# Optimization experiments

Hardware: AMD Instinct MI355X
Metric: run time of the kernel (lower is better)

## Reference

```python
import jax, jax.numpy as jnp
import numpy as np
from jax import lax

V, E, H, K = 50257, 256, 256, 3
T, B, S = 1024, 32, 1024


def setup_inputs() -> dict:
    key = jax.random.key(0)
    ks = jax.random.split(key, 10)
    inp = {
        "source": jax.random.randint(ks[0], (T, B), 0, V),
        "target": jax.random.randint(ks[1], (T, B), 0, V),
        "enc_attn": jax.random.normal(ks[2], (B, S, H), jnp.float32),
        "source_seq_out": jax.random.normal(ks[3], (B, S, 2 * H), jnp.float32),
        "emb": jax.random.normal(ks[4], (V, E), jnp.float32) * 0.02,
        "affine_w": jax.random.normal(ks[5], (2 * H, E), jnp.float32) * 0.02,
        "affine_b": jnp.zeros((2 * H,), jnp.float32),
        "conv_w": jax.random.normal(ks[6], (2 * H, 1, K, 2 * H), jnp.float32) * 0.02,
        "conv_b": jnp.zeros((2 * H,), jnp.float32),
        "map_w": jax.random.normal(ks[7], (2 * H, H), jnp.float32) * 0.02,
        "map_b": jnp.zeros((2 * H,), jnp.float32),
    }
    return inp


def reference(source, target, enc_attn, source_seq_out, emb, affine_w, affine_b,
              conv_w, conv_b, map_w, map_b):
    # source is unused by the original forward (kept for signature fidelity)
    x = emb[target]                                   # [T, B, E]
    x = x @ affine_w.T + affine_b                     # [T, B, 2H]
    x = jnp.transpose(x, (1, 0, 2))                   # [B, T, 2H]  (.t() swaps dims 0,1)
    x = x[:, None, :, :]                              # [B, 1, T, 2H]
    # conv2d: out_ch=2H, kernel=(K, 2H), padding=(K-1, 0) -> [B, 2H, T+K-1, 1]
    y = lax.conv_general_dilated(
        x, conv_w, window_strides=(1, 1),
        padding=((K - 1, K - 1), (0, 0)),
        dimension_numbers=("NCHW", "OIHW", "NCHW"))
    y = y + conv_b[None, :, None, None]
    y = y[:, :, : y.shape[2] - K, :]                  # narrow -> length L = T - 1 (faithful)
    y = jax.nn.relu(y)
    y = jnp.transpose(y[..., 0], (0, 2, 1))           # [B, L, 2H]
    A, Bg = y[..., :H], y[..., H:]                    # GLU split
    dec_attn = A * jax.nn.softmax(Bg, axis=-1)        # [B, L, H]
    dec_attn2 = dec_attn @ map_w.T + map_b            # [B, L, 2H]
    scores = jnp.einsum("blh,bsh->bls", dec_attn, enc_attn)   # [B, L, S]
    attn = jax.nn.softmax(scores, axis=-1)
    attns = jnp.einsum("bls,bsd->bld", attn, source_seq_out)  # [B, L, 2H]
    return dec_attn2 + attns
```

## Files before the change

kernel.cpp:

```cpp
#include <hip/hip_runtime.h>
#include <stdint.h>


typedef __bf16 bf16x8_t __attribute__((ext_vector_type(8)));
typedef float  f32x4_t  __attribute__((ext_vector_type(4)));
typedef unsigned short u16x8 __attribute__((ext_vector_type(8)));

#define DEV __device__ __forceinline__

DEV unsigned short f2bf(float f) {
  union { float f; unsigned u; } v; v.f = f;
  unsigned r = v.u + 0x7fffu + ((v.u >> 16) & 1u);
  return (unsigned short)(r >> 16);
}
DEV float bf2f(unsigned short u) {
  union { unsigned u; float f; } v; v.u = ((unsigned)u) << 16;
  return v.f;
}

DEV void gload_lds16(const void* g, void* l) {
  __builtin_amdgcn_global_load_lds((const __attribute__((address_space(1))) void*)g,
                                   (__attribute__((address_space(3))) void*)l, 16, 0, 0);
}

DEV void vm_bar8() { asm volatile("s_waitcnt vmcnt(8)" ::: "memory"); __builtin_amdgcn_s_barrier(); }
DEV void vm_bar4() { asm volatile("s_waitcnt vmcnt(4)" ::: "memory"); __builtin_amdgcn_s_barrier(); }
DEV void vm_bar0() { asm volatile("s_waitcnt vmcnt(0)" ::: "memory"); __builtin_amdgcn_s_barrier(); }
DEV void lgkm_bar() { asm volatile("s_waitcnt lgkmcnt(0)" ::: "memory"); __builtin_amdgcn_s_barrier(); }

DEV void stage32(unsigned short* Ld, int tid,
                 const unsigned short* a0, const unsigned short* a1,
                 const unsigned short* b0, const unsigned short* b1, int tt) {
  const int o = tt * 32;
  gload_lds16(a0 + o, Ld + tid * 8);
  gload_lds16(a1 + o, Ld + (tid + 256) * 8);
  gload_lds16(b0 + o, Ld + 4096 + tid * 8);
  gload_lds16(b1 + o, Ld + 4096 + (tid + 256) * 8);
}

DEV void gemm_step32(const unsigned short* Ld, int wr, int wc, int ln, int qsw,
                     f32x4_t (&acc)[4][4]) {
  bf16x8_t af[4], bff[4];
#pragma unroll
  for (int x = 0; x < 4; ++x) {
    af[x]  = *(const bf16x8_t*)(Ld + (wr * 64 + x * 16 + ln) * 32 + qsw);
    bff[x] = *(const bf16x8_t*)(Ld + 4096 + (wc * 64 + x * 16 + ln) * 32 + qsw);
  }
  __builtin_amdgcn_s_setprio(1);
#pragma unroll
  for (int mt = 0; mt < 4; ++mt)
#pragma unroll
    for (int nt = 0; nt < 4; ++nt)
      acc[mt][nt] = __builtin_amdgcn_mfma_f32_16x16x32_bf16(af[mt], bff[nt], acc[mt][nt], 0, 0, 0);
  __builtin_amdgcn_s_setprio(0);
}

__global__ void zero_k(unsigned short* p) { p[threadIdx.x] = 0; }

__global__ __launch_bounds__(256) void zero_rows_k(float* p) {
  int i = (blockIdx.x * 256 + threadIdx.x) * 4;
  *(float4*)(p + i) = make_float4(0.f, 0.f, 0.f, 0.f);
}

__global__ __launch_bounds__(256) void cvt_bf16_k(const float* __restrict__ src,
                                                  unsigned short* __restrict__ dst,
                                                  int n) {
  int i = (blockIdx.x * 256 + threadIdx.x) * 4;
  if (i >= n) return;
  float4 v = *(const float4*)(src + i);
  ushort4 o;
  o.x = f2bf(v.x); o.y = f2bf(v.y); o.z = f2bf(v.z); o.w = f2bf(v.w);
  *(ushort4*)(dst + i) = o;
}

__global__ __launch_bounds__(256) void cvt_transpose_v_k(const float* __restrict__ src,
                                                         unsigned short* __restrict__ dst) {
  __shared__ float tile[64][65];
  const int b = blockIdx.z, s0 = blockIdx.x * 64, d0 = blockIdx.y * 64;
  const int tid = threadIdx.x;
  const int cs = (tid & 15) * 4;
  const int rs = tid >> 4;
  const float* p = src + ((size_t)b * 1024 + s0) * 512 + d0;
#pragma unroll
  for (int rr = 0; rr < 4; ++rr) {
    const int s = rs + rr * 16;
    float4 v = *(const float4*)(p + (size_t)s * 512 + cs);
    tile[s][cs] = v.x; tile[s][cs + 1] = v.y;
    tile[s][cs + 2] = v.z; tile[s][cs + 3] = v.w;
  }
  __syncthreads();
  const int ch = tid & 7;
  const int dd0 = tid >> 3;
#pragma unroll
  for (int it = 0; it < 2; ++it) {
    const int dd = dd0 + it * 32;
    u16x8 o;
#pragma unroll
    for (int j = 0; j < 8; ++j) o[j] = f2bf(tile[ch * 8 + j][dd]);
    *(u16x8*)(dst + ((size_t)b * 512 + d0 + dd) * 1024 + s0 + ch * 8) = o;
  }
}

__global__ __launch_bounds__(256) void embed_affine_k(const int* __restrict__ tgt,
                                                      const float* __restrict__ emb,
                                                      const unsigned short* __restrict__ awb,
                                                      const float* __restrict__ ab,
                                                      unsigned short* __restrict__ X) {
  constexpr int AP = 264;
  __shared__ unsigned short xs[32 * AP];
  const int r0 = blockIdx.x * 32;
  const int tid = threadIdx.x;
  for (int idx = tid; idx < 32 * 64; idx += 256) {
    int r = idx >> 6, c4 = (idx & 63) * 4;
    int row = tgt[r0 + r];
    float4 v = *(const float4*)&emb[(size_t)row * 256 + c4];
    ushort4 o;
    o.x = f2bf(v.x); o.y = f2bf(v.y); o.z = f2bf(v.z); o.w = f2bf(v.w);
    *(ushort4*)&xs[r * AP + c4] = o;
  }
  __syncthreads();
  const int lane = tid & 63, w = tid >> 6, q = lane >> 4, ln = lane & 15;
  f32x4_t acc[2][8];
#pragma unroll
  for (int mt = 0; mt < 2; ++mt)
#pragma unroll
    for (int nt = 0; nt < 8; ++nt) acc[mt][nt] = (f32x4_t){0.f, 0.f, 0.f, 0.f};
  for (int kk = 0; kk < 256; kk += 32) {
    bf16x8_t a[2], bb[8];
#pragma unroll
    for (int mt = 0; mt < 2; ++mt)
      a[mt] = *(const bf16x8_t*)(xs + (mt * 16 + ln) * AP + kk + q * 8);
#pragma unroll
    for (int nt = 0; nt < 8; ++nt) {
      int n = ((w * 8 + nt) << 4) + ln;
      bb[nt] = *(const bf16x8_t*)(awb + ((size_t)n << 8) + kk + q * 8);
    }
#pragma unroll
    for (int mt = 0; mt < 2; ++mt)
#pragma unroll
      for (int nt = 0; nt < 8; ++nt)
        acc[mt][nt] = __builtin_amdgcn_mfma_f32_16x16x32_bf16(a[mt], bb[nt], acc[mt][nt], 0, 0, 0);
  }
#pragma unroll
  for (int nt = 0; nt < 8; ++nt) {
    const int o = ((w * 8 + nt) << 4) + ln;
    const float bias = ab[o];
#pragma unroll
    for (int mt = 0; mt < 2; ++mt)
#pragma unroll
      for (int r = 0; r < 4; ++r) {
        int rid = r0 + mt * 16 + q * 4 + r;
        int t = rid >> 5, b = rid & 31;
        X[(((size_t)(b * 1024 + t)) << 9) + o] = f2bf(acc[mt][nt][r] + bias);
      }
  }
}

__global__ __launch_bounds__(256, 3) void conv_gemm_k(const unsigned short* __restrict__ X,
                                                      const unsigned short* __restrict__ Wc,
                                                      const float* __restrict__ cb,
                                                      const unsigned short* __restrict__ zbuf,
                                                      unsigned short* __restrict__ Y) {
  __shared__ unsigned short tb[3][8192];
  const int bid = blockIdx.x;
  const int mtile = ((bid >> 5) << 3) | (bid & 7);
  const int ntile = (bid >> 3) & 3;
  const int b  = mtile >> 3;
  const int l0 = (mtile & 7) << 7;
  const int n0 = ntile << 7;
  const int tid = threadIdx.x;
  const int w = tid >> 6, lane = tid & 63, q = lane >> 4, ln = lane & 15;
  const int wr = w >> 1, wc = w & 1;
  const int qsw = (q ^ (ln & 3)) << 3;

  const int r0g = tid >> 2, r1g = (tid + 256) >> 2;
  const int cg = tid & 3;
  const int c0g = ((cg ^ (r0g & 3)) << 3);
  const int c1g = ((cg ^ (r1g & 3)) << 3);

  const unsigned short* Xb = X + ((size_t)b << 19);
  const int lr0 = l0 + r0g - 2;
  const int lr1 = l0 + r1g - 2;
  const int tmin0 = (lr0 >= 0) ? 0 : (lr0 == -1 ? 16 : 32);
  const unsigned short* a0 = Xb + ((long)lr0 * 512 + c0g);
  const unsigned short* a1 = Xb + ((long)lr1 * 512 + c1g);
  const unsigned short* b0 = Wc + (size_t)(n0 + r0g) * 1536 + c0g;
  const unsigned short* b1 = Wc + (size_t)(n0 + r1g) * 1536 + c1g;

  auto STG = [&](unsigned short* Ld, int tt) {
    const int o = tt * 32;
    const unsigned short* sA0 = (tt >= tmin0) ? (a0 + o) : (zbuf + c0g);
    gload_lds16(sA0, Ld + tid * 8);
    gload_lds16(a1 + o, Ld + (tid + 256) * 8);
    gload_lds16(b0 + o, Ld + 4096 + tid * 8);
    gload_lds16(b1 + o, Ld + 4096 + (tid + 256) * 8);
  };

  f32x4_t acc[4][4];
#pragma unroll
  for (int mt = 0; mt < 4; ++mt)
#pragma unroll
    for (int nt = 0; nt < 4; ++nt) acc[mt][nt] = (f32x4_t){0.f, 0.f, 0.f, 0.f};

  unsigned short *p0 = tb[0], *p1 = tb[1], *p2 = tb[2];
  STG(p0, 0);
  STG(p1, 1);

  for (int t = 0; t < 48; ++t) {
    if (t + 2 < 48) { STG(p2, t + 2); vm_bar8(); }
    else if (t + 1 < 48) vm_bar4();
    else vm_bar0();
    gemm_step32(p0, wr, wc, ln, qsw, acc);
    lgkm_bar();
    unsigned short* tmp = p0; p0 = p1; p1 = p2; p2 = tmp;
  }

#pragma unroll
  for (int nt = 0; nt < 4; ++nt) {
    const int o = n0 + wc * 64 + nt * 16 + ln;
    const float bias = cb[o];
#pragma unroll
    for (int mt = 0; mt < 4; ++mt)
#pragma unroll
      for (int r = 0; r < 4; ++r) {
        const int l = l0 + wr * 64 + mt * 16 + q * 4 + r;
        float v = acc[mt][nt][r] + bias;
        Y[(((size_t)b * 1024 + l) << 9) + o] = f2bf(v > 0.f ? v : 0.f);
      }
  }
}

__global__ __launch_bounds__(256) void glu_k(const unsigned short* __restrict__ Y,
                                             unsigned short* __restrict__ dec) {
  const int row = blockIdx.x * 4 + (threadIdx.x >> 6);
  const int lane = threadIdx.x & 63;
  const unsigned short* p = Y + ((size_t)row << 9);
  ushort4 av = *(const ushort4*)(p + lane * 4);
  ushort4 gv = *(const ushort4*)(p + 256 + lane * 4);
  float e0 = __expf(bf2f(gv.x)), e1 = __expf(bf2f(gv.y));
  float e2 = __expf(bf2f(gv.z)), e3 = __expf(bf2f(gv.w));
  float s = e0 + e1 + e2 + e3;
#pragma unroll
  for (int off = 32; off > 0; off >>= 1) s += __shfl_xor(s, off);
  float inv = 1.f / s;
  ushort4 o;
  o.x = f2bf(bf2f(av.x) * e0 * inv);
  o.y = f2bf(bf2f(av.y) * e1 * inv);
  o.z = f2bf(bf2f(av.z) * e2 * inv);
  o.w = f2bf(bf2f(av.w) * e3 * inv);
  *(ushort4*)(dec + ((size_t)row << 8) + lane * 4) = o;
}

__global__ __launch_bounds__(256, 3) void attn_s_k(const unsigned short* __restrict__ dec,
                                                   const unsigned short* __restrict__ enc,
                                                   unsigned short* __restrict__ P,
                                                   float* __restrict__ rows) {
  __shared__ unsigned short tb[3][8192];
  const int bid = blockIdx.x;
  const int wg = ((bid & 7) << 8) + (bid >> 3);
  const int ntile = wg & 7, mtile = wg >> 3;
  const int b = mtile >> 3;
  const int row0 = mtile << 7;
  const int s0 = ntile << 7;
  const int tid = threadIdx.x;
  const int w = tid >> 6, lane = tid & 63, q = lane >> 4, ln = lane & 15;
  const int wr = w >> 1, wc = w & 1;
  const int qsw = (q ^ (ln & 3)) << 3;

  const int r0g = tid >> 2, r1g = (tid + 256) >> 2;
  const int cg = tid & 3;
  const int c0g = ((cg ^ (r0g & 3)) << 3);
  const int c1g = ((cg ^ (r1g & 3)) << 3);

  const unsigned short* Ab = dec + ((size_t)row0 << 8);
  const unsigned short* Bb = enc + ((size_t)b << 18) + ((size_t)s0 << 8);
  const unsigned short* a0 = Ab + (size_t)r0g * 256 + c0g;
  const unsigned short* a1 = Ab + (size_t)r1g * 256 + c1g;
  const unsigned short* b0 = Bb + (size_t)r0g * 256 + c0g;
  const unsigned short* b1 = Bb + (size_t)r1g * 256 + c1g;

  f32x4_t acc[4][4];
#pragma unroll
  for (int mt = 0; mt < 4; ++mt)
#pragma unroll
    for (int nt = 0; nt < 4; ++nt) acc[mt][nt] = (f32x4_t){0.f, 0.f, 0.f, 0.f};

  unsigned short *p0 = tb[0], *p1 = tb[1], *p2 = tb[2];
  stage32(p0, tid, a0, a1, b0, b1, 0);
  stage32(p1, tid, a0, a1, b0, b1, 1);

  for (int t = 0; t < 8; ++t) {
    if (t + 2 < 8) { stage32(p2, tid, a0, a1, b0, b1, t + 2); vm_bar8(); }
    else if (t + 1 < 8) vm_bar4();
    else vm_bar0();
    gemm_step32(p0, wr, wc, ln, qsw, acc);
    lgkm_bar();
    unsigned short* tmp = p0; p0 = p1; p1 = p2; p2 = tmp;
  }

  float rs[4][4];
#pragma unroll
  for (int mt = 0; mt < 4; ++mt)
#pragma unroll
    for (int r = 0; r < 4; ++r) rs[mt][r] = 0.f;
#pragma unroll
  for (int nt = 0; nt < 4; ++nt) {
    const int col = s0 + wc * 64 + nt * 16 + ln;
#pragma unroll
    for (int mt = 0; mt < 4; ++mt)
#pragma unroll
      for (int r = 0; r < 4; ++r) {
        const int row = row0 + wr * 64 + mt * 16 + q * 4 + r;
        float e = __expf(acc[mt][nt][r]);
        rs[mt][r] += e;
        P[((size_t)row << 10) + col] = f2bf(e);
      }
  }
#pragma unroll
  for (int mt = 0; mt < 4; ++mt)
#pragma unroll
    for (int r = 0; r < 4; ++r) {
      float v = rs[mt][r];
      v += __shfl_xor(v, 1); v += __shfl_xor(v, 2);
      v += __shfl_xor(v, 4); v += __shfl_xor(v, 8);
      if (ln == 0)
        atomicAdd(&rows[row0 + wr * 64 + mt * 16 + q * 4 + r], v);
    }
}

__global__ __launch_bounds__(256, 3) void attn_pv_k(const unsigned short* __restrict__ P,
                                                    const unsigned short* __restrict__ vt,
                                                    const unsigned short* __restrict__ dec,
                                                    const unsigned short* __restrict__ mw,
                                                    const float* __restrict__ rows,
                                                    const float* __restrict__ mb,
                                                    float* __restrict__ out) {
  __shared__ unsigned short tb[3][8192];
  const int bid = blockIdx.x;
  const int wg = ((bid & 7) << 7) + (bid >> 3);
  const int ntile = wg & 3, mtile = wg >> 2;
  const int b = mtile >> 3;
  const int row0 = mtile << 7;
  const int d0 = ntile << 7;
  const int tid = threadIdx.x;
  const int w = tid >> 6, lane = tid & 63, q = lane >> 4, ln = lane & 15;
  const int wr = w >> 1, wc = w & 1;
  const int qsw = (q ^ (ln & 3)) << 3;

  const int r0g = tid >> 2, r1g = (tid + 256) >> 2;
  const int cg = tid & 3;
  const int c0g = ((cg ^ (r0g & 3)) << 3);
  const int c1g = ((cg ^ (r1g & 3)) << 3);

  const unsigned short* A1 = P + ((size_t)row0 << 10);
  const unsigned short* B1 = vt + ((size_t)b << 19) + ((size_t)d0 << 10);
  const unsigned short* A2 = dec + ((size_t)row0 << 8);
  const unsigned short* B2 = mw + ((size_t)d0 << 8);
  const unsigned short* a10 = A1 + (size_t)r0g * 1024 + c0g;
  const unsigned short* a11 = A1 + (size_t)r1g * 1024 + c1g;
  const unsigned short* b10 = B1 + (size_t)r0g * 1024 + c0g;
  const unsigned short* b11 = B1 + (size_t)r1g * 1024 + c1g;
  const unsigned short* a20 = A2 + (size_t)r0g * 256 + c0g;
  const unsigned short* a21 = A2 + (size_t)r1g * 256 + c1g;
  const unsigned short* b20 = B2 + (size_t)r0g * 256 + c0g;
  const unsigned short* b21 = B2 + (size_t)r1g * 256 + c1g;

  auto STG = [&](unsigned short* Ld, int tt) {
    if (tt < 32) stage32(Ld, tid, a10, a11, b10, b11, tt);
    else         stage32(Ld, tid, a20, a21, b20, b21, tt - 32);
  };

  float rinv[4][4];
#pragma unroll
  for (int mt = 0; mt < 4; ++mt)
#pragma unroll
    for (int r = 0; r < 4; ++r)
      rinv[mt][r] = 1.f / rows[row0 + wr * 64 + mt * 16 + q * 4 + r];

  f32x4_t acc[4][4];
#pragma unroll
  for (int mt = 0; mt < 4; ++mt)
#pragma unroll
    for (int nt = 0; nt < 4; ++nt) acc[mt][nt] = (f32x4_t){0.f, 0.f, 0.f, 0.f};

  unsigned short *p0 = tb[0], *p1 = tb[1], *p2 = tb[2];
  STG(p0, 0);
  STG(p1, 1);

  for (int t = 0; t < 32; ++t) {
    STG(p2, t + 2); vm_bar8();
    gemm_step32(p0, wr, wc, ln, qsw, acc);
    lgkm_bar();
    unsigned short* tmp = p0; p0 = p1; p1 = p2; p2 = tmp;
  }
#pragma unroll
  for (int mt = 0; mt < 4; ++mt)
#pragma unroll
    for (int nt = 0; nt < 4; ++nt)
#pragma unroll
      for (int r = 0; r < 4; ++r) acc[mt][nt][r] *= rinv[mt][r];

  for (int t = 32; t < 40; ++t) {
    if (t + 2 < 40) { STG(p2, t + 2); vm_bar8(); }
    else if (t + 1 < 40) vm_bar4();
    else vm_bar0();
    gemm_step32(p0, wr, wc, ln, qsw, acc);
    lgkm_bar();
    unsigned short* tmp = p0; p0 = p1; p1 = p2; p2 = tmp;
  }

#pragma unroll
  for (int nt = 0; nt < 4; ++nt) {
    const int d = d0 + wc * 64 + nt * 16 + ln;
    const float bias = mb[d];
#pragma unroll
    for (int mt = 0; mt < 4; ++mt)
#pragma unroll
      for (int r = 0; r < 4; ++r) {
        const int row = row0 + wr * 64 + mt * 16 + q * 4 + r;
        const int l = row & 1023;
        if (l < 1023)
          out[((size_t)b * 1023 + l) * 512 + d] = acc[mt][nt][r] + bias;
      }
  }
}

extern "C" void kernel_launch(void* const* d_in, const int* in_sizes, int n_in,
                              void* d_out, int out_size, void* d_ws, size_t ws_size,
                              hipStream_t stream) {
  const int*   target = (const int*)d_in[1];
  const float* enc    = (const float*)d_in[2];
  const float* src    = (const float*)d_in[3];
  const float* emb    = (const float*)d_in[4];
  const float* aw     = (const float*)d_in[5];
  const float* ab     = (const float*)d_in[6];
  const float* cw     = (const float*)d_in[7];
  const float* cb     = (const float*)d_in[8];
  const float* mw     = (const float*)d_in[9];
  const float* mb     = (const float*)d_in[10];
  float* out = (float*)d_out;
  char* ws = (char*)d_ws;

  unsigned short* Xbf  = (unsigned short*)(ws);
  unsigned short* Ybf  = (unsigned short*)(ws + 33554432);
  unsigned short* Pb   = (unsigned short*)(ws);
  unsigned short* dec  = (unsigned short*)(ws + 67108864);
  unsigned short* encb = (unsigned short*)(ws + 83886080);
  unsigned short* vtb  = (unsigned short*)(ws + 100663296);
  unsigned short* wcb  = (unsigned short*)(ws + 134217728);
  float*          rows = (float*)(ws + 134217728);
  unsigned short* mwb  = (unsigned short*)(ws + 135790592);
  unsigned short* awb  = (unsigned short*)(ws + 136052736);

  zero_k<<<1, 512, 0, stream>>>(dec);
  cvt_bf16_k<<<8192, 256, 0, stream>>>(enc, encb, 32 * 1024 * 256);
  cvt_bf16_k<<<768, 256, 0, stream>>>(cw, wcb, 512 * 1536);
  cvt_bf16_k<<<128, 256, 0, stream>>>(mw, mwb, 512 * 256);
  cvt_bf16_k<<<128, 256, 0, stream>>>(aw, awb, 512 * 256);
  cvt_transpose_v_k<<<dim3(16, 8, 32), 256, 0, stream>>>(src, vtb);
  embed_affine_k<<<1024, 256, 0, stream>>>(target, emb, awb, ab, Xbf);
  conv_gemm_k<<<1024, 256, 0, stream>>>(Xbf, wcb, cb, dec, Ybf);
  zero_rows_k<<<32, 256, 0, stream>>>(rows);
  glu_k<<<8192, 256, 0, stream>>>(Ybf, dec);
  attn_s_k<<<2048, 256, 0, stream>>>(dec, encb, Pb, rows);
  attn_pv_k<<<1024, 256, 0, stream>>>(Pb, vtb, dec, mwb, rows, mb, out);
}
```

Baseline: 415.6 us.

## Use 256x256 tiles with 8-wave blocks and 4-stage split A/B pipeline

Both conv_gemm_k and attn_pv_k move from 128x128 tiles with 4 waves to 256x256 tiles with 8 waves per block. LDS staging becomes a 4-buffer ring, with the A and B loads issued separately between two MFMA half-steps, and setprio raised around the MFMA bursts. The goal is more operand reuse per global load and better overlap of loads with matrix math. The costs are larger accumulator register use, 256 blocks instead of 1024 (lower occupancy and tail effects on 256 CUs), and extra barriers per k-step.

```diff
diff --git a/kernel.cpp b/kernel.cpp
--- a/kernel.cpp
+++ b/kernel.cpp
@@ -156,63 +156,84 @@
   }
 }
 
-__global__ __launch_bounds__(256, 3) void conv_gemm_k(const unsigned short* __restrict__ X,
+__global__ __launch_bounds__(512, 2) void conv_gemm_k(const unsigned short* __restrict__ X,
                                                       const unsigned short* __restrict__ Wc,
                                                       const float* __restrict__ cb,
                                                       const unsigned short* __restrict__ zbuf,
                                                       unsigned short* __restrict__ Y) {
-  __shared__ unsigned short tb[3][8192];
+  __shared__ unsigned short lds[4][16384];
+  const int tid = threadIdx.x;
+  const int w = tid >> 6, lane = tid & 63, ln = lane & 15, q = lane >> 4;
+  const int wr = w >> 2, wc = w & 3;
+  const int qsw = ((q ^ (ln & 3)) << 3);
+
   const int bid = blockIdx.x;
-  const int mtile = ((bid >> 5) << 3) | (bid & 7);
-  const int ntile = (bid >> 3) & 3;
-  const int b  = mtile >> 3;
-  const int l0 = (mtile & 7) << 7;
-  const int n0 = ntile << 7;
-  const int tid = threadIdx.x;
-  const int w = tid >> 6, lane = tid & 63, q = lane >> 4, ln = lane & 15;
-  const int wr = w >> 1, wc = w & 1;
-  const int qsw = (q ^ (ln & 3)) << 3;
-
-  const int r0g = tid >> 2, r1g = (tid + 256) >> 2;
-  const int cg = tid & 3;
-  const int c0g = ((cg ^ (r0g & 3)) << 3);
-  const int c1g = ((cg ^ (r1g & 3)) << 3);
-
-  const unsigned short* Xb = X + ((size_t)b << 19);
-  const int lr0 = l0 + r0g - 2;
-  const int lr1 = l0 + r1g - 2;
-  const int tmin0 = (lr0 >= 0) ? 0 : (lr0 == -1 ? 16 : 32);
-  const unsigned short* a0 = Xb + ((long)lr0 * 512 + c0g);
-  const unsigned short* a1 = Xb + ((long)lr1 * 512 + c1g);
-  const unsigned short* b0 = Wc + (size_t)(n0 + r0g) * 1536 + c0g;
-  const unsigned short* b1 = Wc + (size_t)(n0 + r1g) * 1536 + c1g;
-
-  auto STG = [&](unsigned short* Ld, int tt) {
-    const int o = tt * 32;
-    const unsigned short* sA0 = (tt >= tmin0) ? (a0 + o) : (zbuf + c0g);
-    gload_lds16(sA0, Ld + tid * 8);
-    gload_lds16(a1 + o, Ld + (tid + 256) * 8);
-    gload_lds16(b0 + o, Ld + 4096 + tid * 8);
-    gload_lds16(b1 + o, Ld + 4096 + (tid + 256) * 8);
+  const int xcd = bid & 7, j = bid >> 3;
+  const int b = ((j >> 3) << 3) + xcd;
+  const int jj = j & 7;
+  const int l0 = (jj >> 1) << 8;
+  const int n0 = (jj & 1) << 8;
+
+  const int R = tid >> 2, cg = tid & 3;
+  const int sw = ((cg ^ (R & 3)) << 3);
+  const unsigned short* aP0 = X + ((long)(b * 1024 + l0 + R - 2) * 512 + sw);
+  const unsigned short* aP1 = aP0 + (long)128 * 512;
+  const unsigned short* bP0 = Wc + ((long)(n0 + R) * 1536 + sw);
+  const unsigned short* bP1 = bP0 + (long)128 * 1536;
+  const int tmin0 = (l0 == 0) ? (R == 0 ? 32 : (R == 1 ? 16 : 0)) : 0;
+
+  auto STGA = [&](int tkt) {
+    unsigned short* Ld = lds[tkt & 3];
+    const unsigned short* s0 = (tkt >= tmin0) ? (aP0 + tkt * 32) : (zbuf + sw);
+    gload_lds16(s0, Ld + tid * 8);
+    gload_lds16(aP1 + tkt * 32, Ld + 4096 + tid * 8);
   };
-
-  f32x4_t acc[4][4];
-#pragma unroll
-  for (int mt = 0; mt < 4; ++mt)
+  auto STGB = [&](int tkt) {
+    unsigned short* Ld = lds[tkt & 3];
+    gload_lds16(bP0 + tkt * 32, Ld + 8192 + tid * 8);
+    gload_lds16(bP1 + tkt * 32, Ld + 12288 + tid * 8);
+  };
+
+  f32x4_t acc[8][4];
+#pragma unroll
+  for (int mt = 0; mt < 8; ++mt)
 #pragma unroll
     for (int nt = 0; nt < 4; ++nt) acc[mt][nt] = (f32x4_t){0.f, 0.f, 0.f, 0.f};
 
-  unsigned short *p0 = tb[0], *p1 = tb[1], *p2 = tb[2];
-  STG(p0, 0);
-  STG(p1, 1);
-
-  for (int t = 0; t < 48; ++t) {
-    if (t + 2 < 48) { STG(p2, t + 2); vm_bar8(); }
-    else if (t + 1 < 48) vm_bar4();
-    else vm_bar0();
-    gemm_step32(p0, wr, wc, ln, qsw, acc);
-    lgkm_bar();
-    unsigned short* tmp = p0; p0 = p1; p1 = p2; p2 = tmp;
+  STGA(0); STGB(0); STGA(1); STGB(1);
+
+  for (int kt = 0; kt < 48; ++kt) {
+    if (kt < 47) asm volatile("s_waitcnt vmcnt(4)" ::: "memory");
+    else         asm volatile("s_waitcnt vmcnt(0)" ::: "memory");
+    __builtin_amdgcn_s_barrier();
+    const unsigned short* Ld = lds[kt & 3];
+    bf16x8_t af[4], bff[4];
+#pragma unroll
+    for (int x = 0; x < 4; ++x) {
+      af[x]  = *(const bf16x8_t*)(Ld + (wr * 128 + x * 16 + ln) * 32 + qsw);
+      bff[x] = *(const bf16x8_t*)(Ld + 8192 + (wc * 64 + x * 16 + ln) * 32 + qsw);
+    }
+    if (kt < 46) STGA(kt + 2);
+    __builtin_amdgcn_s_setprio(1);
+#pragma unroll
+    for (int mt = 0; mt < 4; ++mt)
+#pragma unroll
+      for (int nt = 0; nt < 4; ++nt)
+        acc[mt][nt] = __builtin_amdgcn_mfma_f32_16x16x32_bf16(af[mt], bff[nt], acc[mt][nt], 0, 0, 0);
+    __builtin_amdgcn_s_setprio(0);
+    __builtin_amdgcn_s_barrier();
+#pragma unroll
+    for (int x = 0; x < 4; ++x)
+      af[x] = *(const bf16x8_t*)(Ld + (wr * 128 + 64 + x * 16 + ln) * 32 + qsw);
+    if (kt < 46) STGB(kt + 2);
+    __builtin_amdgcn_s_setprio(1);
+#pragma unroll
+    for (int mt = 0; mt < 4; ++mt)
+#pragma unroll
+      for (int nt = 0; nt < 4; ++nt)
+        acc[4 + mt][nt] = __builtin_amdgcn_mfma_f32_16x16x32_bf16(af[mt], bff[nt], acc[4 + mt][nt], 0, 0, 0);
+    __builtin_amdgcn_s_setprio(0);
+    __builtin_amdgcn_s_barrier();
   }
 
 #pragma unroll
@@ -220,10 +241,10 @@
     const int o = n0 + wc * 64 + nt * 16 + ln;
     const float bias = cb[o];
 #pragma unroll
-    for (int mt = 0; mt < 4; ++mt)
+    for (int mt = 0; mt < 8; ++mt)
 #pragma unroll
       for (int r = 0; r < 4; ++r) {
-        const int l = l0 + wr * 64 + mt * 16 + q * 4 + r;
+        const int l = l0 + wr * 128 + mt * 16 + q * 4 + r;
         float v = acc[mt][nt][r] + bias;
         Y[(((size_t)b * 1024 + l) << 9) + o] = f2bf(v > 0.f ? v : 0.f);
       }
@@ -328,85 +349,113 @@
     }
 }
 
-__global__ __launch_bounds__(256, 3) void attn_pv_k(const unsigned short* __restrict__ P,
+__global__ __launch_bounds__(512, 2) void attn_pv_k(const unsigned short* __restrict__ P,
                                                     const unsigned short* __restrict__ vt,
                                                     const unsigned short* __restrict__ dec,
                                                     const unsigned short* __restrict__ mw,
                                                     const float* __restrict__ rows,
                                                     const float* __restrict__ mb,
                                                     float* __restrict__ out) {
-  __shared__ unsigned short tb[3][8192];
+  __shared__ unsigned short lds[4][16384];
+  const int tid = threadIdx.x;
+  const int w = tid >> 6, lane = tid & 63, ln = lane & 15, q = lane >> 4;
+  const int wr = w >> 2, wc = w & 3;
+  const int qsw = ((q ^ (ln & 3)) << 3);
+
   const int bid = blockIdx.x;
-  const int wg = ((bid & 7) << 7) + (bid >> 3);
-  const int ntile = wg & 3, mtile = wg >> 2;
-  const int b = mtile >> 3;
-  const int row0 = mtile << 7;
-  const int d0 = ntile << 7;
-  const int tid = threadIdx.x;
-  const int w = tid >> 6, lane = tid & 63, q = lane >> 4, ln = lane & 15;
-  const int wr = w >> 1, wc = w & 1;
-  const int qsw = (q ^ (ln & 3)) << 3;
-
-  const int r0g = tid >> 2, r1g = (tid + 256) >> 2;
-  const int cg = tid & 3;
-  const int c0g = ((cg ^ (r0g & 3)) << 3);
-  const int c1g = ((cg ^ (r1g & 3)) << 3);
-
-  const unsigned short* A1 = P + ((size_t)row0 << 10);
-  const unsigned short* B1 = vt + ((size_t)b << 19) + ((size_t)d0 << 10);
-  const unsigned short* A2 = dec + ((size_t)row0 << 8);
-  const unsigned short* B2 = mw + ((size_t)d0 << 8);
-  const unsigned short* a10 = A1 + (size_t)r0g * 1024 + c0g;
-  const unsigned short* a11 = A1 + (size_t)r1g * 1024 + c1g;
-  const unsigned short* b10 = B1 + (size_t)r0g * 1024 + c0g;
-  const unsigned short* b11 = B1 + (size_t)r1g * 1024 + c1g;
-  const unsigned short* a20 = A2 + (size_t)r0g * 256 + c0g;
-  const unsigned short* a21 = A2 + (size_t)r1g * 256 + c1g;
-  const unsigned short* b20 = B2 + (size_t)r0g * 256 + c0g;
-  const unsigned short* b21 = B2 + (size_t)r1g * 256 + c1g;
-
-  auto STG = [&](unsigned short* Ld, int tt) {
-    if (tt < 32) stage32(Ld, tid, a10, a11, b10, b11, tt);
-    else         stage32(Ld, tid, a20, a21, b20, b21, tt - 32);
+  const int xcd = bid & 7, j = bid >> 3;
+  const int b = ((j >> 3) << 3) + xcd;
+  const int jj = j & 7;
+  const int row0 = b * 1024 + ((jj >> 1) << 8);
+  const int d0 = (jj & 1) << 8;
+
+  const int R = tid >> 2, cg = tid & 3;
+  const int sw = ((cg ^ (R & 3)) << 3);
+  const unsigned short* a1P0 = P + ((long)(row0 + R) * 1024 + sw);
+  const unsigned short* a1P1 = a1P0 + (long)128 * 1024;
+  const unsigned short* b1P0 = vt + ((long)b << 19) + ((long)(d0 + R) * 1024 + sw);
+  const unsigned short* b1P1 = b1P0 + (long)128 * 1024;
+  const unsigned short* a2P0 = dec + ((long)(row0 + R) * 256 + sw);
+  const unsigned short* a2P1 = a2P0 + (long)128 * 256;
+  const unsigned short* b2P0 = mw + ((long)(d0 + R) * 256 + sw);
+  const unsigned short* b2P1 = b2P0 + (long)128 * 256;
+
+  auto STGA = [&](int tkt) {
+    unsigned short* Ld = lds[tkt & 3];
+    if (tkt < 32) {
+      gload_lds16(a1P0 + tkt * 32, Ld + tid * 8);
+      gload_lds16(a1P1 + tkt * 32, Ld + 4096 + tid * 8);
+    } else {
+      gload_lds16(a2P0 + (tkt - 32) * 32, Ld + tid * 8);
+      gload_lds16(a2P1 + (tkt - 32) * 32, Ld + 4096 + tid * 8);
+    }
   };
-
-  float rinv[4][4];
-#pragma unroll
-  for (int mt = 0; mt < 4; ++mt)
+  auto STGB = [&](int tkt) {
+    unsigned short* Ld = lds[tkt & 3];
+    if (tkt < 32) {
+      gload_lds16(b1P0 + tkt * 32, Ld + 8192 + tid * 8);
+      gload_lds16(b1P1 + tkt * 32, Ld + 12288 + tid * 8);
+    } else {
+      gload_lds16(b2P0 + (tkt - 32) * 32, Ld + 8192 + tid * 8);
+      gload_lds16(b2P1 + (tkt - 32) * 32, Ld + 12288 + tid * 8);
+    }
+  };
+
+  float rinv[8][4];
+#pragma unroll
+  for (int mt = 0; mt < 8; ++mt)
 #pragma unroll
     for (int r = 0; r < 4; ++r)
-      rinv[mt][r] = 1.f / rows[row0 + wr * 64 + mt * 16 + q * 4 + r];
-
-  f32x4_t acc[4][4];
-#pragma unroll
-  for (int mt = 0; mt < 4; ++mt)
+      rinv[mt][r] = 1.f / rows[row0 + wr * 128 + mt * 16 + q * 4 + r];
+
+  f32x4_t acc[8][4];
+#pragma unroll
+  for (int mt = 0; mt < 8; ++mt)
 #pragma unroll
     for (int nt = 0; nt < 4; ++nt) acc[mt][nt] = (f32x4_t){0.f, 0.f, 0.f, 0.f};
 
-  unsigned short *p0 = tb[0], *p1 = tb[1], *p2 = tb[2];
-  STG(p0, 0);
-  STG(p1, 1);
-
-  for (int t = 0; t < 32; ++t) {
-    STG(p2, t + 2); vm_bar8();
-    gemm_step32(p0, wr, wc, ln, qsw, acc);
-    lgkm_bar();
-    unsigned short* tmp = p0; p0 = p1; p1 = p2; p2 = tmp;
-  }
-#pragma unroll
-  for (int mt = 0; mt < 4; ++mt)
-#pragma unroll
-    for (int nt = 0; nt < 4; ++nt)
-#pragma unroll
-      for (int r = 0; r < 4; ++r) acc[mt][nt][r] *= rinv[mt][r];
-
-  for (int t = 32; t < 40; ++t) {
-    if (t + 2 < 40) { STG(p2, t + 2); vm_bar8(); }
-    else if (t + 1 < 40) vm_bar4();
-    else vm_bar0();
-    gemm_step32(p0, wr, wc, ln, qsw, acc);
-    lgkm_bar();
-    unsigned short* tmp = p0; p0 = p1; p1 = p2; p2 = tmp;
+  STGA(0); STGB(0); STGA(1); STGB(1);
+
+  for (int kt = 0; kt < 40; ++kt) {
+    if (kt < 39) asm volatile("s_waitcnt vmcnt(4)" ::: "memory");
+    else         asm volatile("s_waitcnt vmcnt(0)" ::: "memory");
+    __builtin_amdgcn_s_barrier();
+    const unsigned short* Ld = lds[kt & 3];
+    bf16x8_t af[4], bff[4];
+#pragma unroll
+    for (int x = 0; x < 4; ++x) {
+      af[x]  = *(const bf16x8_t*)(Ld + (wr * 128 + x * 16 + ln) * 32 + qsw);
+      bff[x] = *(const bf16x8_t*)(Ld + 8192 + (wc * 64 + x * 16 + ln) * 32 + qsw);
+    }
+    if (kt < 38) STGA(kt + 2);
+    __builtin_amdgcn_s_setprio(1);
+#pragma unroll
+    for (int mt = 0; mt < 4; ++mt)
+#pragma unroll
+      for (int nt = 0; nt < 4; ++nt)
+        acc[mt][nt] = __builtin_amdgcn_mfma_f32_16x16x32_bf16(af[mt], bff[nt], acc[mt][nt], 0, 0, 0);
+    __builtin_amdgcn_s_setprio(0);
+    __builtin_amdgcn_s_barrier();
+#pragma unroll
+    for (int x = 0; x < 4; ++x)
+      af[x] = *(const bf16x8_t*)(Ld + (wr * 128 + 64 + x * 16 + ln) * 32 + qsw);
+    if (kt < 38) STGB(kt + 2);
+    __builtin_amdgcn_s_setprio(1);
+#pragma unroll
+    for (int mt = 0; mt < 4; ++mt)
+#pragma unroll
+      for (int nt = 0; nt < 4; ++nt)
+        acc[4 + mt][nt] = __builtin_amdgcn_mfma_f32_16x16x32_bf16(af[mt], bff[nt], acc[4 + mt][nt], 0, 0, 0);
+    __builtin_amdgcn_s_setprio(0);
+    __builtin_amdgcn_s_barrier();
+    if (kt == 31) {
+#pragma unroll
+      for (int mt = 0; mt < 8; ++mt)
+#pragma unroll
+        for (int nt = 0; nt < 4; ++nt)
+#pragma unroll
+          for (int r = 0; r < 4; ++r) acc[mt][nt][r] *= rinv[mt][r];
+    }
   }
 
 #pragma unroll
@@ -414,10 +463,10 @@
     const int d = d0 + wc * 64 + nt * 16 + ln;
     const float bias = mb[d];
 #pragma unroll
-    for (int mt = 0; mt < 4; ++mt)
+    for (int mt = 0; mt < 8; ++mt)
 #pragma unroll
       for (int r = 0; r < 4; ++r) {
-        const int row = row0 + wr * 64 + mt * 16 + q * 4 + r;
+        const int row = row0 + wr * 128 + mt * 16 + q * 4 + r;
         const int l = row & 1023;
         if (l < 1023)
           out[((size_t)b * 1023 + l) * 512 + d] = acc[mt][nt][r] + bias;
@@ -459,9 +508,9 @@
   cvt_bf16_k<<<128, 256, 0, stream>>>(aw, awb, 512 * 256);
   cvt_transpose_v_k<<<dim3(16, 8, 32), 256, 0, stream>>>(src, vtb);
   embed_affine_k<<<1024, 256, 0, stream>>>(target, emb, awb, ab, Xbf);
-  conv_gemm_k<<<1024, 256, 0, stream>>>(Xbf, wcb, cb, dec, Ybf);
+  conv_gemm_k<<<256, 512, 0, stream>>>(Xbf, wcb, cb, dec, Ybf);
   zero_rows_k<<<32, 256, 0, stream>>>(rows);
   glu_k<<<8192, 256, 0, stream>>>(Ybf, dec);
   attn_s_k<<<2048, 256, 0, stream>>>(dec, encb, Pb, rows);
-  attn_pv_k<<<1024, 256, 0, stream>>>(Pb, vtb, dec, mwb, rows, mb, out);
-}
+  attn_pv_k<<<256, 512, 0, stream>>>(Pb, vtb, dec, mwb, rows, mb, out);
+}
```

New measurement: 412.2 us. No clear change (-0.8%).
